# Performance work log

Hardware: AMD Instinct MI355X
Metric: run time of the kernel (lower is better)

Reference implementation:

```python
import jax, jax.numpy as jnp
import numpy as np

B, T, C, H = 512, 4096, 7, 3  # batch, time, 7 classes, 3 heads


def setup_inputs() -> dict:
    key = jax.random.key(0)
    k0, k1, k2, k3, k4, k5 = jax.random.split(key, 6)
    # outputs are treated as probabilities (log is taken directly); keep them in (0.01, 1]
    mk_out = lambda k: jax.random.uniform(k, (B, T, C), dtype=jnp.float32, minval=0.01, maxval=1.0)
    return {
        "out0": mk_out(k0),
        "out1": mk_out(k1),
        "out2": mk_out(k2),
        "labels_3": jax.random.randint(k3, (B, T, H), 0, C, dtype=jnp.int64),
        "mask": jax.random.uniform(k4, (B, T), dtype=jnp.float32),
        "reward": jax.random.uniform(k5, (B, T, H), dtype=jnp.float32),
    }


def reference(out0, out1, out2, labels_3, mask, reward):
    N = B * T
    outs = jnp.stack([out0, out1, out2], axis=0).reshape(H, N, C)   # [3, N, 7]
    labels = labels_3.reshape(N, H).T                               # [3, N]
    rw = reward.reshape(N, H).T                                     # [3, N]
    valid = mask.reshape(N) < 0.5                                   # [N] bool
    n_valid = valid.sum()

    # gather probability of the true class per head: op[h, n] = outs[h, n, labels[h, n]]
    op = jnp.take_along_axis(outs, labels[:, :, None], axis=2)[..., 0]  # [3, N]
    # original: sum_h -dot(log(op_h), sr_h) / n_valid  (n_valid identical across heads)
    loss = -jnp.where(valid[None, :], jnp.log(op) * rw, 0.0).sum() / n_valid

    pred = jnp.argmax(outs, axis=-1)                                # [3, N]
    correct = jnp.all(pred == labels, axis=0) & valid               # product over heads on valid positions
    n_correct = correct.sum()
    return loss, n_correct, n_valid
```

## Files before the change

kernel.cpp:

```cpp
#include <hip/hip_runtime.h>

constexpr long long N_ROWS = 512LL * 4096LL;
constexpr int BLOCK   = 256;
constexpr int CHUNK   = 256;
constexpr int CPB     = 4;
constexpr int NBLOCKS = (int)(N_ROWS / ((long long)CHUNK * CPB));

constexpr int BUF_WORDS = 7168;

__device__ __forceinline__ void async16(const float* g, float* l) {
    __builtin_amdgcn_global_load_lds(
        (const __attribute__((address_space(1))) unsigned int*)g,
        (__attribute__((address_space(3))) unsigned int*)l,
        16, 0, 0);
}

__global__ __launch_bounds__(BLOCK) void shortloss_main(
    const float* __restrict__ out0,
    const float* __restrict__ out1,
    const float* __restrict__ out2,
    const int*   __restrict__ labels,
    const float* __restrict__ mask,
    const float* __restrict__ reward,
    float4*      __restrict__ partials)
{
    __shared__ float lds[2 * BUF_WORDS];
    const int tid = threadIdx.x;
    const long long c0 = (long long)blockIdx.x * CPB;
    const float* outs[3] = {out0, out1, out2};

    auto stage = [&](long long c, int b) {
        float* buf = lds + b * BUF_WORDS;
        #pragma unroll
        for (int h = 0; h < 3; ++h) {
            const float* src = outs[h] + c * (CHUNK * 7);
            float*       dst = buf + h * 1792;
            async16(src + 4 * (size_t)tid, dst + 4 * tid);
            if (tid < 192)
                async16(src + 4 * (size_t)(256 + tid), dst + 4 * (256 + tid));
        }
        if (tid < 192) {
            async16((const float*)(labels) + c * (CHUNK * 3) + 4 * (size_t)tid, buf + 5376 + 4 * tid);
            async16(reward + c * (CHUNK * 3) + 4 * (size_t)tid,                 buf + 6144 + 4 * tid);
        }
        if (tid < 64)
            async16(mask + c * CHUNK + 4 * (size_t)tid, buf + 6912 + 4 * tid);
    };

    float L = 0.0f;
    int   C = 0, V = 0;

    auto compute = [&](int b) {
        const float* buf  = lds + b * BUF_WORDS;
        const int*   labp = (const int*)(buf + 5376);
        const bool valid = buf[6912 + tid] < 0.5f;
        V += valid ? 1 : 0;
        int   ok   = 1;
        float lsum = 0.0f;
        #pragma unroll
        for (int h = 0; h < 3; ++h) {
            const int lbl = labp[tid * 3 + h];
            const float* vr = buf + h * 1792 + tid * 7;
            float v[7];
            #pragma unroll
            for (int cc = 0; cc < 7; ++cc) v[cc] = vr[cc];

            float best = v[0]; int bestc = 0;
            #pragma unroll
            for (int cc = 1; cc < 7; ++cc)
                if (v[cc] > best) { best = v[cc]; bestc = cc; }

            float opv = v[0];
            #pragma unroll
            for (int cc = 1; cc < 7; ++cc)
                opv = (lbl == cc) ? v[cc] : opv;

            lsum += __logf(opv) * buf[6144 + tid * 3 + h];
            ok &= (bestc == lbl) ? 1 : 0;
        }
        L += valid ? lsum : 0.0f;
        C += (valid && ok) ? 1 : 0;
    };

    stage(c0, 0);
    __syncthreads();
    #pragma unroll
    for (int k = 0; k < CPB; ++k) {
        if (k + 1 < CPB) stage(c0 + k + 1, (k + 1) & 1);
        compute(k & 1);
        __syncthreads();
    }

    #pragma unroll
    for (int off = 32; off > 0; off >>= 1) {
        L += __shfl_down(L, off, 64);
        C += __shfl_down(C, off, 64);
        V += __shfl_down(V, off, 64);
    }
    __shared__ float sL[BLOCK / 64];
    __shared__ int   sC[BLOCK / 64], sV[BLOCK / 64];
    const int wave = tid >> 6;
    if ((tid & 63) == 0) { sL[wave] = L; sC[wave] = C; sV[wave] = V; }
    __syncthreads();
    if (tid == 0) {
        float l = 0.0f; int cc = 0, vv = 0;
        #pragma unroll
        for (int w = 0; w < BLOCK / 64; ++w) { l += sL[w]; cc += sC[w]; vv += sV[w]; }
        partials[blockIdx.x] = make_float4(l, (float)cc, (float)vv, 0.0f);
    }
}

__global__ __launch_bounds__(256) void shortloss_reduce(
    const float4* __restrict__ partials,
    float* __restrict__ out)
{
    float L = 0.0f, C = 0.0f, V = 0.0f;
    for (int i = threadIdx.x; i < NBLOCKS; i += 256) {
        float4 p = partials[i];
        L += p.x; C += p.y; V += p.z;
    }
    #pragma unroll
    for (int off = 32; off > 0; off >>= 1) {
        L += __shfl_down(L, off, 64);
        C += __shfl_down(C, off, 64);
        V += __shfl_down(V, off, 64);
    }
    __shared__ float sL[4], sC[4], sV[4];
    const int wave = threadIdx.x >> 6;
    if ((threadIdx.x & 63) == 0) { sL[wave] = L; sC[wave] = C; sV[wave] = V; }
    __syncthreads();
    if (threadIdx.x == 0) {
        float l = 0.0f, c = 0.0f, v = 0.0f;
        #pragma unroll
        for (int w = 0; w < 4; ++w) { l += sL[w]; c += sC[w]; v += sV[w]; }
        out[0] = -l / v;
        out[1] = c;
        out[2] = v;
    }
}

extern "C" void kernel_launch(void* const* d_in, const int* in_sizes, int n_in,
                              void* d_out, int out_size, void* d_ws, size_t ws_size,
                              hipStream_t stream) {
    const float* out0   = (const float*)d_in[0];
    const float* out1   = (const float*)d_in[1];
    const float* out2   = (const float*)d_in[2];
    const int*   labels = (const int*)  d_in[3];
    const float* mask   = (const float*)d_in[4];
    const float* reward = (const float*)d_in[5];

    float4* partials = (float4*)d_ws;

    shortloss_main<<<NBLOCKS, BLOCK, 0, stream>>>(
        out0, out1, out2, labels, mask, reward, partials);
    shortloss_reduce<<<1, 256, 0, stream>>>(partials, (float*)d_out);
}
```

Measured before the change: 226.5 us.

## Replace LDS double-buffered async staging with direct per-thread float4 global loads

Drops the global-to-LDS async copy pipeline and its barriers. Each thread now handles four consecutive rows and reads outputs, labels, rewards and mask straight into registers as vectorized float4/int4 loads. This removes LDS traffic and synchronisation, but each thread's loads are strided by 112 bytes across lanes, which reduces coalescing per instruction and raises register pressure (28 floats per head). Launch bounds now request four blocks per CU.

```diff
diff --git a/kernel.cpp b/kernel.cpp
--- a/kernel.cpp
+++ b/kernel.cpp
@@ -1,21 +1,11 @@
 #include <hip/hip_runtime.h>
 
 constexpr long long N_ROWS = 512LL * 4096LL;
-constexpr int BLOCK   = 256;
-constexpr int CHUNK   = 256;
-constexpr int CPB     = 4;
-constexpr int NBLOCKS = (int)(N_ROWS / ((long long)CHUNK * CPB));
+constexpr int BLOCK = 256;
+constexpr int RPT   = 4;
+constexpr int NBLOCKS = (int)(N_ROWS / ((long long)BLOCK * RPT));
 
-constexpr int BUF_WORDS = 7168;
-
-__device__ __forceinline__ void async16(const float* g, float* l) {
-    __builtin_amdgcn_global_load_lds(
-        (const __attribute__((address_space(1))) unsigned int*)g,
-        (__attribute__((address_space(3))) unsigned int*)l,
-        16, 0, 0);
-}
-
-__global__ __launch_bounds__(BLOCK) void shortloss_main(
+__global__ __launch_bounds__(BLOCK, 4) void shortloss_main(
     const float* __restrict__ out0,
     const float* __restrict__ out1,
     const float* __restrict__ out2,
@@ -24,46 +14,48 @@
     const float* __restrict__ reward,
     float4*      __restrict__ partials)
 {
-    __shared__ float lds[2 * BUF_WORDS];
     const int tid = threadIdx.x;
-    const long long c0 = (long long)blockIdx.x * CPB;
+    const long long g = (long long)blockIdx.x * BLOCK + tid;
+
     const float* outs[3] = {out0, out1, out2};
 
-    auto stage = [&](long long c, int b) {
-        float* buf = lds + b * BUF_WORDS;
+    float4 mkv = ((const float4*)mask)[g];
+    const float mk[4] = {mkv.x, mkv.y, mkv.z, mkv.w};
+
+    int lb[12];
+    {
+        const int4* lp = (const int4*)labels;
         #pragma unroll
-        for (int h = 0; h < 3; ++h) {
-            const float* src = outs[h] + c * (CHUNK * 7);
-            float*       dst = buf + h * 1792;
-            async16(src + 4 * (size_t)tid, dst + 4 * tid);
-            if (tid < 192)
-                async16(src + 4 * (size_t)(256 + tid), dst + 4 * (256 + tid));
+        for (int j = 0; j < 3; ++j) {
+            int4 t = lp[3 * g + j];
+            lb[4*j+0] = t.x; lb[4*j+1] = t.y; lb[4*j+2] = t.z; lb[4*j+3] = t.w;
         }
-        if (tid < 192) {
-            async16((const float*)(labels) + c * (CHUNK * 3) + 4 * (size_t)tid, buf + 5376 + 4 * tid);
-            async16(reward + c * (CHUNK * 3) + 4 * (size_t)tid,                 buf + 6144 + 4 * tid);
+    }
+    float rw[12];
+    {
+        const float4* rp = (const float4*)reward;
+        #pragma unroll
+        for (int j = 0; j < 3; ++j) {
+            float4 t = rp[3 * g + j];
+            rw[4*j+0] = t.x; rw[4*j+1] = t.y; rw[4*j+2] = t.z; rw[4*j+3] = t.w;
         }
-        if (tid < 64)
-            async16(mask + c * CHUNK + 4 * (size_t)tid, buf + 6912 + 4 * tid);
-    };
+    }
 
-    float L = 0.0f;
-    int   C = 0, V = 0;
-
-    auto compute = [&](int b) {
-        const float* buf  = lds + b * BUF_WORDS;
-        const int*   labp = (const int*)(buf + 5376);
-        const bool valid = buf[6912 + tid] < 0.5f;
-        V += valid ? 1 : 0;
-        int   ok   = 1;
-        float lsum = 0.0f;
+    float lsum[4] = {0.f, 0.f, 0.f, 0.f};
+    int   ok[4]   = {1, 1, 1, 1};
+    #pragma unroll
+    for (int h = 0; h < 3; ++h) {
+        float o[28];
+        const float4* op = (const float4*)outs[h];
         #pragma unroll
-        for (int h = 0; h < 3; ++h) {
-            const int lbl = labp[tid * 3 + h];
-            const float* vr = buf + h * 1792 + tid * 7;
-            float v[7];
-            #pragma unroll
-            for (int cc = 0; cc < 7; ++cc) v[cc] = vr[cc];
+        for (int j = 0; j < 7; ++j) {
+            float4 t = op[7 * g + j];
+            o[4*j+0] = t.x; o[4*j+1] = t.y; o[4*j+2] = t.z; o[4*j+3] = t.w;
+        }
+        #pragma unroll
+        for (int i = 0; i < 4; ++i) {
+            const int lbl = lb[3*i + h];
+            const float* v = o + 7*i;
 
             float best = v[0]; int bestc = 0;
             #pragma unroll
@@ -75,20 +67,19 @@
             for (int cc = 1; cc < 7; ++cc)
                 opv = (lbl == cc) ? v[cc] : opv;
 
-            lsum += __logf(opv) * buf[6144 + tid * 3 + h];
-            ok &= (bestc == lbl) ? 1 : 0;
+            lsum[i] += __logf(opv) * rw[3*i + h];
+            ok[i]   &= (bestc == lbl) ? 1 : 0;
         }
-        L += valid ? lsum : 0.0f;
-        C += (valid && ok) ? 1 : 0;
-    };
+    }
 
-    stage(c0, 0);
-    __syncthreads();
+    float L = 0.0f;
+    int   C = 0, V = 0;
     #pragma unroll
-    for (int k = 0; k < CPB; ++k) {
-        if (k + 1 < CPB) stage(c0 + k + 1, (k + 1) & 1);
-        compute(k & 1);
-        __syncthreads();
+    for (int i = 0; i < 4; ++i) {
+        const bool valid = mk[i] < 0.5f;
+        V += valid ? 1 : 0;
+        L += valid ? lsum[i] : 0.0f;
+        C += (valid && ok[i]) ? 1 : 0;
     }
 
     #pragma unroll
```

After: 227.6 us. No clear change (+0.5%).

## Specialize waves for staging and use partial vmcnt waits for real double buffering

Applied to the files above, without the earlier changes.

Reassigns async global-to-LDS staging so waves 0-2 each load one head's probabilities and wave 3 loads labels, reward and mask, seven 16-byte loads per lane. Replaces __syncthreads with an explicit vmcnt(7) wait plus raw s_barrier, so the next chunk's loads stay in flight while the current chunk is computed. Also doubles chunks per block, halving the grid. The intent is to overlap memory latency with compute instead of draining all loads at each barrier. It relies on every wave issuing exactly seven loads per stage for the vmcnt count to be correct, and the larger CPB reduces block count and parallelism.

```diff
diff --git a/kernel.cpp b/kernel.cpp
--- a/kernel.cpp
+++ b/kernel.cpp
@@ -1,12 +1,12 @@
 #include <hip/hip_runtime.h>
 
 constexpr long long N_ROWS = 512LL * 4096LL;
-constexpr int BLOCK   = 256;
-constexpr int CHUNK   = 256;
-constexpr int CPB     = 4;
+constexpr int BLOCK = 256;
+constexpr int CHUNK = 256;
+constexpr int CPB   = 8;
 constexpr int NBLOCKS = (int)(N_ROWS / ((long long)CHUNK * CPB));
 
-constexpr int BUF_WORDS = 7168;
+constexpr int BUFW = 7168;
 
 __device__ __forceinline__ void async16(const float* g, float* l) {
     __builtin_amdgcn_global_load_lds(
@@ -14,6 +14,12 @@
         (__attribute__((address_space(3))) unsigned int*)l,
         16, 0, 0);
 }
+
+#define BARRIER() do {                       \
+    asm volatile("" ::: "memory");           \
+    __builtin_amdgcn_s_barrier();            \
+    asm volatile("" ::: "memory");           \
+} while (0)
 
 __global__ __launch_bounds__(BLOCK) void shortloss_main(
     const float* __restrict__ out0,
@@ -24,43 +30,49 @@
     const float* __restrict__ reward,
     float4*      __restrict__ partials)
 {
-    __shared__ float lds[2 * BUF_WORDS];
+    __shared__ float lds[2 * BUFW];
     const int tid = threadIdx.x;
+    const int wv  = tid >> 6;
+    const int ln  = tid & 63;
     const long long c0 = (long long)blockIdx.x * CPB;
     const float* outs[3] = {out0, out1, out2};
 
     auto stage = [&](long long c, int b) {
-        float* buf = lds + b * BUF_WORDS;
-        #pragma unroll
-        for (int h = 0; h < 3; ++h) {
-            const float* src = outs[h] + c * (CHUNK * 7);
-            float*       dst = buf + h * 1792;
-            async16(src + 4 * (size_t)tid, dst + 4 * tid);
-            if (tid < 192)
-                async16(src + 4 * (size_t)(256 + tid), dst + 4 * (256 + tid));
+        float* buf = lds + b * BUFW;
+        if (wv < 3) {
+            const float* src = outs[wv] + c * 1792;
+            float*       dst = buf + wv * 1792;
+            #pragma unroll
+            for (int j = 0; j < 7; ++j)
+                async16(src + j * 256 + 4 * (size_t)ln, dst + j * 256 + 4 * ln);
+        } else {
+            const float* lsrc = (const float*)labels + c * 768;
+            const float* rsrc = reward + c * 768;
+            #pragma unroll
+            for (int j = 0; j < 3; ++j)
+                async16(lsrc + j * 256 + 4 * (size_t)ln, buf + 5376 + j * 256 + 4 * ln);
+            #pragma unroll
+            for (int j = 0; j < 3; ++j)
+                async16(rsrc + j * 256 + 4 * (size_t)ln, buf + 6144 + j * 256 + 4 * ln);
+            async16(mask + c * 256 + 4 * (size_t)ln, buf + 6912 + 4 * ln);
         }
-        if (tid < 192) {
-            async16((const float*)(labels) + c * (CHUNK * 3) + 4 * (size_t)tid, buf + 5376 + 4 * tid);
-            async16(reward + c * (CHUNK * 3) + 4 * (size_t)tid,                 buf + 6144 + 4 * tid);
-        }
-        if (tid < 64)
-            async16(mask + c * CHUNK + 4 * (size_t)tid, buf + 6912 + 4 * tid);
     };
 
     float L = 0.0f;
     int   C = 0, V = 0;
 
     auto compute = [&](int b) {
-        const float* buf  = lds + b * BUF_WORDS;
+        const float* buf  = lds + b * BUFW;
         const int*   labp = (const int*)(buf + 5376);
-        const bool valid = buf[6912 + tid] < 0.5f;
+        const int r = (wv << 6) + ln;
+        const bool valid = buf[6912 + r] < 0.5f;
         V += valid ? 1 : 0;
         int   ok   = 1;
         float lsum = 0.0f;
         #pragma unroll
         for (int h = 0; h < 3; ++h) {
-            const int lbl = labp[tid * 3 + h];
-            const float* vr = buf + h * 1792 + tid * 7;
+            const int lbl = labp[r * 3 + h];
+            const float* vr = buf + h * 1792 + r * 7;
             float v[7];
             #pragma unroll
             for (int cc = 0; cc < 7; ++cc) v[cc] = vr[cc];
@@ -75,7 +87,7 @@
             for (int cc = 1; cc < 7; ++cc)
                 opv = (lbl == cc) ? v[cc] : opv;
 
-            lsum += __logf(opv) * buf[6144 + tid * 3 + h];
+            lsum += __logf(opv) * buf[6144 + r * 3 + h];
             ok &= (bestc == lbl) ? 1 : 0;
         }
         L += valid ? lsum : 0.0f;
@@ -83,12 +95,17 @@
     };
 
     stage(c0, 0);
-    __syncthreads();
     #pragma unroll
     for (int k = 0; k < CPB; ++k) {
-        if (k + 1 < CPB) stage(c0 + k + 1, (k + 1) & 1);
+        if (k + 1 < CPB) {
+            stage(c0 + k + 1, (k + 1) & 1);
+            asm volatile("s_waitcnt vmcnt(7)" ::: "memory");
+        } else {
+            asm volatile("s_waitcnt vmcnt(0)" ::: "memory");
+        }
+        BARRIER();
         compute(k & 1);
-        __syncthreads();
+        BARRIER();
     }
 
     #pragma unroll
@@ -99,8 +116,7 @@
     }
     __shared__ float sL[BLOCK / 64];
     __shared__ int   sC[BLOCK / 64], sV[BLOCK / 64];
-    const int wave = tid >> 6;
-    if ((tid & 63) == 0) { sL[wave] = L; sC[wave] = C; sV[wave] = V; }
+    if (ln == 0) { sL[wv] = L; sC[wv] = C; sV[wv] = V; }
     __syncthreads();
     if (tid == 0) {
         float l = 0.0f; int cc = 0, vv = 0;
```

After: 226.3 us. No clear change (-0.1%).
